# Performance work log

Hardware: AMD Instinct MI355X
Metric: run time of the kernel (lower is better)

Reference implementation:

```python
import jax, jax.numpy as jnp
import numpy as np

D = 64       # hidden_dim
ED = 16      # edge_dim
N = 50000
E = 400000
T = 2
STEP = 0.5   # euler fixed step over t in [0,1] -> 2 steps
EPS = 1e-5

def setup_inputs() -> dict:
    key = jax.random.key(0)
    ks = jax.random.split(key, 14)
    def lin(k, fi, fo):
        return jax.random.normal(k, (fi, fo), jnp.float32) / np.sqrt(fi)
    return {
        'h_seq': jax.random.normal(ks[0], (T, N, D), jnp.float32),
        'edge_attr': jax.random.normal(ks[1], (T, E, ED), jnp.float32),
        # msg_net: MLP(2D+ED -> D -> D), 2 layers with ReLU
        'W1': lin(ks[2], 2 * D + ED, D), 'b1': jnp.zeros((D,), jnp.float32),
        'W2': lin(ks[3], D, D),          'b2': jnp.zeros((D,), jnp.float32),
        # dynamics_net: Linear(2D,D) -> LayerNorm -> SiLU -> Linear(D,D) -> Tanh
        'Wd1': lin(ks[4], 2 * D, D), 'bd1': jnp.zeros((D,), jnp.float32),
        'ln_g': jnp.ones((D,), jnp.float32), 'ln_b': jnp.zeros((D,), jnp.float32),
        'Wd2': lin(ks[5], D, D), 'bd2': jnp.zeros((D,), jnp.float32),
        'edge_index': jax.random.randint(ks[6], (T, 2, E), 0, N, jnp.int32),
    }

def _ode_func(h, row, col, ea, W1, b1, W2, b2, Wd1, bd1, ln_g, ln_b, Wd2, bd2):
    # identity transport: Q_uv @ h_v == h_v
    h_transported = h[col]                              # [E, D]
    msg_in = jnp.concatenate([h[row], h_transported, ea], axis=-1)  # [E, 2D+ED]
    msg = jax.nn.relu(msg_in @ W1 + b1) @ W2 + b2       # [E, D]
    agg = jax.ops.segment_sum(msg, row, num_segments=h.shape[0])    # [N, D]
    x = jnp.concatenate([h, agg], axis=-1) @ Wd1 + bd1  # [N, D]
    mu = x.mean(-1, keepdims=True)
    var = x.var(-1, keepdims=True)
    x = (x - mu) * jax.lax.rsqrt(var + EPS) * ln_g + ln_b
    x = jax.nn.silu(x) @ Wd2 + bd2
    return jnp.tanh(x)

def reference(h_seq, edge_attr, W1, b1, W2, b2, Wd1, bd1, ln_g, ln_b, Wd2, bd2, edge_index):
    params = (W1, b1, W2, b2, Wd1, bd1, ln_g, ln_b, Wd2, bd2)
    n_steps = int(round(1.0 / STEP))
    h_prev = h_seq[0]
    disagreements = []
    for t in range(T):
        row, col = edge_index[t, 0], edge_index[t, 1]
        ea = edge_attr[t]
        h = h_prev + h_seq[t]                           # h_fused
        for _ in range(n_steps):                        # fixed-step Euler
            h = h + STEP * _ode_func(h, row, col, ea, *params)
        diff = h[row] - h[col]                          # Q=I -> h_u - h_v
        disagreements.append(jnp.minimum((diff * diff).sum(-1), 1e4))
        h_prev = h
    return h_prev, jnp.stack(disagreements)             # h_final [N,D], D [T,E]
```

## Files before the change

kernel.cpp:

```cpp
#include <hip/hip_runtime.h>

#define NN 50000
#define EE 400000
#define NT64 6250
#define EGRID 1250
#define NBLK 782
#define SBLK 49

typedef __bf16 bf16x8 __attribute__((ext_vector_type(8)));
typedef float f32x4 __attribute__((ext_vector_type(4)));

static __device__ __forceinline__ ushort f2bf(float f) {
    union { float f; unsigned int i; } x; x.f = f;
    unsigned int r = x.i + 0x7fffu + ((x.i >> 16) & 1u);
    return (ushort)(r >> 16);
}
static __device__ __forceinline__ float bf2f(ushort u) {
    union { unsigned int i; float f; } x; x.i = ((unsigned int)u) << 16; return x.f;
}
static __device__ __forceinline__ unsigned pack2(float lo, float hi) {
    return (unsigned)f2bf(lo) | ((unsigned)f2bf(hi) << 16);
}
static __device__ __forceinline__ float fast_tanh(float x) {
    float e = __expf(2.f * x);
    return 1.f - 2.f / (e + 1.f);
}
static __device__ __forceinline__ bf16x8 pk8(float4 f0, float4 f1) {
    union { uint4 u; bf16x8 v; } z;
    z.u = make_uint4(pack2(f0.x, f0.y), pack2(f0.z, f0.w),
                     pack2(f1.x, f1.y), pack2(f1.z, f1.w));
    return z.v;
}
static __device__ __forceinline__ bf16x8 zero8() {
    union { uint4 u; bf16x8 v; } z;
    z.u = make_uint4(0u, 0u, 0u, 0u);
    return z.v;
}

__global__ __launch_bounds__(256) void prep_edge_k(
    const float* __restrict__ W1, const float* __restrict__ W2,
    const float* __restrict__ b1, const float* __restrict__ b2,
    ushort* __restrict__ B1P, ushort* __restrict__ B2P,
    float* __restrict__ b1f, float* __restrict__ b2f)
{
    int idx = blockIdx.x * 256 + threadIdx.x;
    if (idx < 10240) {
        int j = idx & 7, n = (idx >> 3) & 63, qk = idx >> 9;
        int kc = qk >> 2, quad = qk & 3;
        int k = kc * 32 + quad * 8 + j;
        B1P[idx] = (k < 144) ? f2bf(W1[k * 64 + n]) : (ushort)0;
    }
    if (idx < 4096) {
        int j = idx & 7, n = (idx >> 3) & 63, qk = idx >> 9;
        int kc = qk >> 2, quad = qk & 3;
        int k = kc * 32 + quad * 8 + j;
        B2P[idx] = f2bf(W2[k * 64 + n]);
    }
    if (idx < 64) { b1f[idx] = b1[idx]; b2f[idx] = b2[idx]; }
}

__global__ __launch_bounds__(256) void prep_node_k(
    const float* __restrict__ Wd1, const float* __restrict__ Wd2,
    const float* __restrict__ bd1, const float* __restrict__ lng,
    const float* __restrict__ lnb, const float* __restrict__ bd2,
    ushort* __restrict__ Wd1P, ushort* __restrict__ Wd2P,
    float* __restrict__ bd1f, float* __restrict__ lngf,
    float* __restrict__ lnbf, float* __restrict__ bd2f)
{
    int idx = blockIdx.x * 256 + threadIdx.x;
    if (idx < 8192) {
        int j = idx & 7, n = (idx >> 3) & 63, qk = idx >> 9;
        int kc = qk >> 2, quad = qk & 3;
        int k = kc * 32 + quad * 8 + j;
        Wd1P[idx] = f2bf(Wd1[k * 64 + n]);
    }
    if (idx < 4096) {
        int j = idx & 7, n = (idx >> 3) & 63, qk = idx >> 9;
        int kc = qk >> 2, quad = qk & 3;
        int k = kc * 32 + quad * 8 + j;
        Wd2P[idx] = f2bf(Wd2[k * 64 + n]);
    }
    if (idx < 64) {
        bd1f[idx] = bd1[idx]; lngf[idx] = lng[idx];
        lnbf[idx] = lnb[idx]; bd2f[idx] = bd2[idx];
    }
}

__global__ __launch_bounds__(256) void state_k(
    float* __restrict__ h, ushort* __restrict__ hb,
    const float* __restrict__ hseq_t, int mode)
{
    int i = blockIdx.x * 256 + threadIdx.x;
    float v = hseq_t[i];
    float r = (mode == 0) ? (2.f * v) : (h[i] + v);
    h[i] = r; hb[i] = f2bf(r);
}

__global__ __launch_bounds__(256) void zero_k(int* __restrict__ p, int n) {
    int i = blockIdx.x * 256 + threadIdx.x;
    if (i < n) p[i] = 0;
}
__global__ __launch_bounds__(256) void zero_f(float* __restrict__ p) {
    int i = blockIdx.x * 256 + threadIdx.x;
    p[i] = 0.f;
}
__global__ __launch_bounds__(256) void hist_k(const int* __restrict__ ei, int* __restrict__ counts) {
    int e = blockIdx.x * 256 + threadIdx.x;
    const int* rows = ei + (size_t)blockIdx.y * 2 * EE;
    int* cnt = counts + blockIdx.y * NN;
    if (e < EE) atomicAdd(&cnt[rows[e]], 1);
}
__global__ __launch_bounds__(256) void scanA_k(
    const int* __restrict__ counts_, int* __restrict__ offsets_, int* __restrict__ bsum_)
{
    const int* counts = counts_ + blockIdx.y * NN;
    int* offsets = offsets_ + blockIdx.y * (NN + 1);
    int* bsum = bsum_ + blockIdx.y * 64;
    __shared__ int wsum[4];
    int tid = threadIdx.x, lane = tid & 63, w = tid >> 6;
    int i4 = blockIdx.x * 1024 + tid * 4;
    int4 v = make_int4(0, 0, 0, 0);
    if (i4 + 3 < NN) v = *(const int4*)(counts + i4);
    else {
        if (i4 < NN) v.x = counts[i4];
        if (i4 + 1 < NN) v.y = counts[i4 + 1];
        if (i4 + 2 < NN) v.z = counts[i4 + 2];
    }
    int s = v.x + v.y + v.z + v.w;
    int x = s;
    for (int off = 1; off < 64; off <<= 1) {
        int y = __shfl_up(x, off);
        if (lane >= off) x += y;
    }
    if (lane == 63) wsum[w] = x;
    __syncthreads();
    int wpre = 0;
    for (int j = 0; j < w; j++) wpre += wsum[j];
    int excl = wpre + x - s;
    int e0 = excl, e1 = e0 + v.x, e2 = e1 + v.y, e3 = e2 + v.z;
    if (i4 + 3 < NN) *(int4*)(offsets + i4) = make_int4(e0, e1, e2, e3);
    else {
        if (i4 < NN) offsets[i4] = e0;
        if (i4 + 1 < NN) offsets[i4 + 1] = e1;
        if (i4 + 2 < NN) offsets[i4 + 2] = e2;
    }
    if (tid == 255) bsum[blockIdx.x] = wpre + x;
}
__global__ __launch_bounds__(256) void scanC_k(
    int* __restrict__ offsets_, const int* __restrict__ bsum_, int* __restrict__ cursor_)
{
    int* offsets = offsets_ + blockIdx.y * (NN + 1);
    const int* bsum = bsum_ + blockIdx.y * 64;
    int* cursor = cursor_ + blockIdx.y * NN;
    int i = blockIdx.x * 256 + threadIdx.x;
    if (i < NN) {
        int b = i >> 10;
        int add = 0;
        for (int j = 0; j < b; j++) add += bsum[j];
        int o = offsets[i] + add;
        offsets[i] = o; cursor[i] = o;
    }
    if (i == 0) offsets[NN] = EE;
}
__global__ __launch_bounds__(256) void fill_idx_k(
    const int* __restrict__ ei, int* __restrict__ cursor_, int* __restrict__ esort_)
{
    int e = blockIdx.x * 256 + threadIdx.x;
    const int* rows = ei + (size_t)blockIdx.y * 2 * EE;
    int* cursor = cursor_ + blockIdx.y * NN;
    int* esort = esort_ + (size_t)blockIdx.y * EE;
    if (e < EE) {
        int p = atomicAdd(&cursor[rows[e]], 1);
        if ((unsigned)p < (unsigned)EE) esort[p] = e;
    }
}

__global__ __launch_bounds__(256) void gather_k(
    const int* __restrict__ esort, const int* __restrict__ rows,
    const int* __restrict__ cols, const float* __restrict__ ea,
    int* __restrict__ rsort, int* __restrict__ csort, ushort* __restrict__ eab)
{
    int p = blockIdx.x * 256 + threadIdx.x;
    if (p < EE) {
        int e = esort[p];
        rsort[p] = rows[e];
        csort[p] = cols[e];
        const float* sp = ea + (size_t)e * 16;
        float4 f0 = ((const float4*)sp)[0], f1 = ((const float4*)sp)[1];
        float4 f2 = ((const float4*)sp)[2], f3 = ((const float4*)sp)[3];
        uint4* dp = (uint4*)(eab + (size_t)p * 16);
        dp[0] = make_uint4(pack2(f0.x, f0.y), pack2(f0.z, f0.w),
                           pack2(f1.x, f1.y), pack2(f1.z, f1.w));
        dp[1] = make_uint4(pack2(f2.x, f2.y), pack2(f2.z, f2.w),
                           pack2(f3.x, f3.y), pack2(f3.z, f3.w));
    }
}

__global__ __launch_bounds__(256, 5) void edge_k(
    const ushort* __restrict__ hb,
    const int* __restrict__ ridx, const int* __restrict__ cidx,
    const ushort* __restrict__ eab,
    const ushort* __restrict__ B1P, const ushort* __restrict__ B2P,
    const float* __restrict__ b1f, const float* __restrict__ b2f,
    ushort* __restrict__ msg)
{
    __shared__ __attribute__((aligned(16))) ushort sB1[10240];
    __shared__ __attribute__((aligned(16))) ushort sH[64 * 72];

    int tid = threadIdx.x;
    int lane = tid & 63, wave = tid >> 6;
    int m = lane & 15, quad = lane >> 4;

    for (int i = tid; i < 10240 / 8; i += 256) ((uint4*)sB1)[i] = ((const uint4*)B1P)[i];
    bf16x8 b2r[2][4];
    for (int kc = 0; kc < 2; kc++)
        for (int nt = 0; nt < 4; nt++)
            b2r[kc][nt] = *(const bf16x8*)(B2P + ((kc * 4 + quad) * 64 + nt * 16 + m) * 8);
    float b1v[4], b2v[4];
    for (int nt = 0; nt < 4; nt++) { b1v[nt] = b1f[nt * 16 + m]; b2v[nt] = b2f[nt * 16 + m]; }
    __syncthreads();

    ushort* sHw = sH + wave * 1152;
    int sl = wave * 16 + m;
    int t0 = blockIdx.x * 5;

    int rc = ridx[t0 * 64 + sl], cc = cidx[t0 * 64 + sl];
    bf16x8 aC[5];
    aC[0] = *(const bf16x8*)(hb + (size_t)rc * 64 + quad * 8);
    aC[1] = *(const bf16x8*)(hb + (size_t)rc * 64 + 32 + quad * 8);
    aC[2] = *(const bf16x8*)(hb + (size_t)cc * 64 + quad * 8);
    aC[3] = *(const bf16x8*)(hb + (size_t)cc * 64 + 32 + quad * 8);
    aC[4] = zero8();
    if (quad < 2) aC[4] = *(const bf16x8*)(eab + (size_t)(t0 * 64 + sl) * 16 + quad * 8);
    int rn = ridx[(t0 + 1) * 64 + sl], cn = cidx[(t0 + 1) * 64 + sl];

    for (int t = t0; t < t0 + 5; t++) {
        int tn = (t + 1 < t0 + 5) ? t + 1 : t;
        bf16x8 aN[5];
        aN[0] = *(const bf16x8*)(hb + (size_t)rn * 64 + quad * 8);
        aN[1] = *(const bf16x8*)(hb + (size_t)rn * 64 + 32 + quad * 8);
        aN[2] = *(const bf16x8*)(hb + (size_t)cn * 64 + quad * 8);
        aN[3] = *(const bf16x8*)(hb + (size_t)cn * 64 + 32 + quad * 8);
        aN[4] = zero8();
        if (quad < 2) aN[4] = *(const bf16x8*)(eab + (size_t)(tn * 64 + sl) * 16 + quad * 8);
        int tnn = (t + 2 < t0 + 5) ? t + 2 : t;
        int rn2 = ridx[tnn * 64 + sl], cn2 = cidx[tnn * 64 + sl];

        f32x4 acc[4];
        #pragma unroll
        for (int nt = 0; nt < 4; nt++) acc[nt] = (f32x4){0.f, 0.f, 0.f, 0.f};
        #pragma unroll
        for (int kc = 0; kc < 5; kc++) {
            #pragma unroll
            for (int nt = 0; nt < 4; nt++) {
                bf16x8 b = *(const bf16x8*)(sB1 + ((kc * 4 + quad) * 64 + nt * 16 + m) * 8);
                acc[nt] = __builtin_amdgcn_mfma_f32_16x16x32_bf16(aC[kc], b, acc[nt], 0, 0, 0);
            }
        }

        __builtin_amdgcn_wave_barrier();
        #pragma unroll
        for (int nt = 0; nt < 4; nt++) {
            int colid = nt * 16 + m;
            float bb = b1v[nt];
            #pragma unroll
            for (int rr = 0; rr < 4; rr++) {
                float v = acc[nt][rr] + bb;
                v = v > 0.f ? v : 0.f;
                sHw[(quad * 4 + rr) * 72 + colid] = f2bf(v);
            }
        }
        __builtin_amdgcn_wave_barrier();

        f32x4 acc2[4];
        #pragma unroll
        for (int nt = 0; nt < 4; nt++) acc2[nt] = (f32x4){0.f, 0.f, 0.f, 0.f};
        #pragma unroll
        for (int kc = 0; kc < 2; kc++) {
            bf16x8 av = *(const bf16x8*)(sHw + m * 72 + kc * 32 + quad * 8);
            #pragma unroll
            for (int nt = 0; nt < 4; nt++) {
                acc2[nt] = __builtin_amdgcn_mfma_f32_16x16x32_bf16(av, b2r[kc][nt], acc2[nt], 0, 0, 0);
            }
        }

        #pragma unroll
        for (int nt = 0; nt < 4; nt++) {
            int colid = nt * 16 + m;
            float bb = b2v[nt];
            #pragma unroll
            for (int rr = 0; rr < 4; rr++) {
                int so = t * 64 + wave * 16 + quad * 4 + rr;
                msg[(size_t)so * 64 + colid] = f2bf(acc2[nt][rr] + bb);
            }
        }

        #pragma unroll
        for (int k2 = 0; k2 < 5; k2++) aC[k2] = aN[k2];
        rn = rn2; cn = cn2;
    }
}

__global__ __launch_bounds__(256, 5) void nodeagg_k(
    float* __restrict__ h, ushort* __restrict__ hbm,
    const ushort* __restrict__ msg, const int* __restrict__ offsets,
    const ushort* __restrict__ Wd1P, const ushort* __restrict__ Wd2P,
    const float* __restrict__ bd1f, const float* __restrict__ lngf,
    const float* __restrict__ lnbf, const float* __restrict__ bd2f)
{
    __shared__ __attribute__((aligned(16))) float aggL[64][68];
    __shared__ __attribute__((aligned(16))) ushort sX[64 * 72];
    int tid = threadIdx.x;
    int lane = tid & 63, wave = tid >> 6;
    int m = lane & 15, quad = lane >> 4;
    int nbase = blockIdx.x * 64;

    for (int idx = wave; idx < 64; idx += 4) {
        int n = nbase + idx;
        float a = 0.f;
        if (n < NN) {
            int bgn = offsets[n], end2 = offsets[n + 1];
            int i = bgn;
            for (; i + 4 <= end2; i += 4) {
                a += bf2f(msg[(size_t)i * 64 + lane]);
                a += bf2f(msg[(size_t)(i + 1) * 64 + lane]);
                a += bf2f(msg[(size_t)(i + 2) * 64 + lane]);
                a += bf2f(msg[(size_t)(i + 3) * 64 + lane]);
            }
            for (; i < end2; i++) a += bf2f(msg[(size_t)i * 64 + lane]);
        }
        aggL[idx][lane] = a;
    }

    float gA[4], bA[4], d1[4], d2[4];
    for (int nt = 0; nt < 4; nt++) {
        int f = nt * 16 + m;
        d1[nt] = bd1f[f]; gA[nt] = lngf[f]; bA[nt] = lnbf[f]; d2[nt] = bd2f[f];
    }
    __syncthreads();

    int n_true = nbase + wave * 16 + m;
    bool own = (n_true < NN);
    int n = own ? n_true : (NN - 1);
    int nl = wave * 16 + m;
    bf16x8 A[4];
    A[0] = *(const bf16x8*)(hbm + (size_t)n * 64 + quad * 8);
    A[1] = *(const bf16x8*)(hbm + (size_t)n * 64 + 32 + quad * 8);
    {
        float4 g0 = *(const float4*)&aggL[nl][quad * 8];
        float4 g1 = *(const float4*)&aggL[nl][quad * 8 + 4];
        float4 g2 = *(const float4*)&aggL[nl][32 + quad * 8];
        float4 g3 = *(const float4*)&aggL[nl][32 + quad * 8 + 4];
        A[2] = pk8(g0, g1);
        A[3] = pk8(g2, g3);
    }

    f32x4 acc[4];
    #pragma unroll
    for (int nt = 0; nt < 4; nt++) acc[nt] = (f32x4){0.f, 0.f, 0.f, 0.f};
    #pragma unroll
    for (int kc = 0; kc < 4; kc++) {
        #pragma unroll
        for (int nt = 0; nt < 4; nt++) {
            bf16x8 b = *(const bf16x8*)(Wd1P + ((kc * 4 + quad) * 64 + nt * 16 + m) * 8);
            acc[nt] = __builtin_amdgcn_mfma_f32_16x16x32_bf16(A[kc], b, acc[nt], 0, 0, 0);
        }
    }

    float xs[4][4];
    #pragma unroll
    for (int nt = 0; nt < 4; nt++)
        #pragma unroll
        for (int r = 0; r < 4; r++)
            xs[nt][r] = acc[nt][r] + d1[nt];

    ushort* sXw = sX + wave * 1152;
    #pragma unroll
    for (int r = 0; r < 4; r++) {
        float s1 = 0.f, s2 = 0.f;
        #pragma unroll
        for (int nt = 0; nt < 4; nt++) { float v = xs[nt][r]; s1 += v; s2 += v * v; }
        for (int off = 1; off < 16; off <<= 1) {
            s1 += __shfl_xor(s1, off);
            s2 += __shfl_xor(s2, off);
        }
        float mean = s1 * (1.f / 64.f);
        float var = fmaxf(s2 * (1.f / 64.f) - mean * mean, 0.f);
        float rstd = rsqrtf(var + 1e-5f);
        #pragma unroll
        for (int nt = 0; nt < 4; nt++) {
            float xn = (xs[nt][r] - mean) * rstd * gA[nt] + bA[nt];
            float slv = xn / (1.f + __expf(-xn));
            sXw[(quad * 4 + r) * 72 + nt * 16 + m] = f2bf(slv);
        }
    }
    __builtin_amdgcn_wave_barrier();

    f32x4 acc2[4];
    #pragma unroll
    for (int nt = 0; nt < 4; nt++) acc2[nt] = (f32x4){0.f, 0.f, 0.f, 0.f};
    #pragma unroll
    for (int kc = 0; kc < 2; kc++) {
        bf16x8 av = *(const bf16x8*)(sXw + m * 72 + kc * 32 + quad * 8);
        #pragma unroll
        for (int nt = 0; nt < 4; nt++) {
            bf16x8 b = *(const bf16x8*)(Wd2P + ((kc * 4 + quad) * 64 + nt * 16 + m) * 8);
            acc2[nt] = __builtin_amdgcn_mfma_f32_16x16x32_bf16(av, b, acc2[nt], 0, 0, 0);
        }
    }

    #pragma unroll
    for (int r = 0; r < 4; r++) {
        int g = nbase + wave * 16 + quad * 4 + r;
        if (g < NN) {
            #pragma unroll
            for (int nt = 0; nt < 4; nt++) {
                int f = nt * 16 + m;
                float y = fast_tanh(acc2[nt][r] + d2[nt]);
                float hn = h[(size_t)g * 64 + f] + 0.5f * y;
                h[(size_t)g * 64 + f] = hn;
                hbm[(size_t)g * 64 + f] = f2bf(hn);
            }
        }
    }
}

__global__ __launch_bounds__(256, 5) void edge_fb_k(
    const ushort* __restrict__ hb,
    const int* __restrict__ ridx, const int* __restrict__ cidx,
    const float* __restrict__ eaf,
    const ushort* __restrict__ B1P, const ushort* __restrict__ B2P,
    const float* __restrict__ b1f, const float* __restrict__ b2f,
    float* __restrict__ agg)
{
    __shared__ __attribute__((aligned(16))) ushort sB1[10240];
    __shared__ __attribute__((aligned(16))) ushort sH[64 * 72];

    int tid = threadIdx.x;
    int lane = tid & 63, wave = tid >> 6;
    int m = lane & 15, quad = lane >> 4;

    for (int i = tid; i < 10240 / 8; i += 256) ((uint4*)sB1)[i] = ((const uint4*)B1P)[i];
    bf16x8 b2r[2][4];
    for (int kc = 0; kc < 2; kc++)
        for (int nt = 0; nt < 4; nt++)
            b2r[kc][nt] = *(const bf16x8*)(B2P + ((kc * 4 + quad) * 64 + nt * 16 + m) * 8);
    float b1v[4], b2v[4];
    for (int nt = 0; nt < 4; nt++) { b1v[nt] = b1f[nt * 16 + m]; b2v[nt] = b2f[nt * 16 + m]; }
    __syncthreads();

    ushort* sHw = sH + wave * 1152;
    int sl = wave * 16 + m;
    int t0 = blockIdx.x * 5;

    for (int t = t0; t < t0 + 5; t++) {
        int s = t * 64 + sl;
        int r = ridx[s], c = cidx[s];
        bf16x8 a[5];
        a[0] = *(const bf16x8*)(hb + (size_t)r * 64 + quad * 8);
        a[1] = *(const bf16x8*)(hb + (size_t)r * 64 + 32 + quad * 8);
        a[2] = *(const bf16x8*)(hb + (size_t)c * 64 + quad * 8);
        a[3] = *(const bf16x8*)(hb + (size_t)c * 64 + 32 + quad * 8);
        a[4] = zero8();
        if (quad < 2) {
            const float* sp = eaf + (size_t)s * 16 + quad * 8;
            a[4] = pk8(((const float4*)sp)[0], ((const float4*)sp)[1]);
        }
        f32x4 acc[4];
        #pragma unroll
        for (int nt = 0; nt < 4; nt++) acc[nt] = (f32x4){0.f, 0.f, 0.f, 0.f};
        #pragma unroll
        for (int kc = 0; kc < 5; kc++)
            #pragma unroll
            for (int nt = 0; nt < 4; nt++) {
                bf16x8 b = *(const bf16x8*)(sB1 + ((kc * 4 + quad) * 64 + nt * 16 + m) * 8);
                acc[nt] = __builtin_amdgcn_mfma_f32_16x16x32_bf16(a[kc], b, acc[nt], 0, 0, 0);
            }
        __builtin_amdgcn_wave_barrier();
        #pragma unroll
        for (int nt = 0; nt < 4; nt++) {
            float bb = b1v[nt];
            #pragma unroll
            for (int rr = 0; rr < 4; rr++) {
                float v = acc[nt][rr] + bb;
                v = v > 0.f ? v : 0.f;
                sHw[(quad * 4 + rr) * 72 + nt * 16 + m] = f2bf(v);
            }
        }
        __builtin_amdgcn_wave_barrier();
        f32x4 acc2[4];
        #pragma unroll
        for (int nt = 0; nt < 4; nt++) acc2[nt] = (f32x4){0.f, 0.f, 0.f, 0.f};
        #pragma unroll
        for (int kc = 0; kc < 2; kc++) {
            bf16x8 av = *(const bf16x8*)(sHw + m * 72 + kc * 32 + quad * 8);
            #pragma unroll
            for (int nt = 0; nt < 4; nt++)
                acc2[nt] = __builtin_amdgcn_mfma_f32_16x16x32_bf16(av, b2r[kc][nt], acc2[nt], 0, 0, 0);
        }
        int base = t * 64 + wave * 16 + quad * 4;
        int r0 = ridx[base], r1 = ridx[base + 1], r2 = ridx[base + 2], r3 = ridx[base + 3];
        #pragma unroll
        for (int nt = 0; nt < 4; nt++) {
            int colid = nt * 16 + m;
            float bb = b2v[nt];
            float v0 = acc2[nt][0] + bb, v1 = acc2[nt][1] + bb;
            float v2 = acc2[nt][2] + bb, v3 = acc2[nt][3] + bb;
            float sum = v0; int pr = r0;
            if (r1 == pr) sum += v1;
            else { atomicAdd(&agg[(size_t)pr * 64 + colid], sum); pr = r1; sum = v1; }
            if (r2 == pr) sum += v2;
            else { atomicAdd(&agg[(size_t)pr * 64 + colid], sum); pr = r2; sum = v2; }
            if (r3 == pr) sum += v3;
            else { atomicAdd(&agg[(size_t)pr * 64 + colid], sum); pr = r3; sum = v3; }
            atomicAdd(&agg[(size_t)pr * 64 + colid], sum);
        }
    }
}

__global__ __launch_bounds__(256, 4) void node_k(
    float* __restrict__ h, ushort* __restrict__ hbm,
    float* __restrict__ agg,
    const ushort* __restrict__ Wd1P, const ushort* __restrict__ Wd2P,
    const float* __restrict__ bd1f, const float* __restrict__ lngf,
    const float* __restrict__ lnbf, const float* __restrict__ bd2f)
{
    __shared__ __attribute__((aligned(16))) ushort sB1[8192];
    __shared__ __attribute__((aligned(16))) ushort sB2[4096];
    __shared__ __attribute__((aligned(16))) ushort sX[64 * 72];
    int tid = threadIdx.x;
    int lane = tid & 63, wave = tid >> 6;
    int m = lane & 15, quad = lane >> 4;
    int nbase = blockIdx.x * 64;

    for (int i = tid; i < 8192 / 8; i += 256) ((uint4*)sB1)[i] = ((const uint4*)Wd1P)[i];
    for (int i = tid; i < 4096 / 8; i += 256) ((uint4*)sB2)[i] = ((const uint4*)Wd2P)[i];
    float gA[4], bA[4], d1[4], d2[4];
    for (int nt = 0; nt < 4; nt++) {
        int f = nt * 16 + m;
        d1[nt] = bd1f[f]; gA[nt] = lngf[f]; bA[nt] = lnbf[f]; d2[nt] = bd2f[f];
    }
    __syncthreads();

    int n_true = nbase + wave * 16 + m;
    bool own = (n_true < NN);
    int n = own ? n_true : (NN - 1);
    bf16x8 A[4];
    A[0] = *(const bf16x8*)(hbm + (size_t)n * 64 + quad * 8);
    A[1] = *(const bf16x8*)(hbm + (size_t)n * 64 + 32 + quad * 8);
    {
        const float* ap = agg + (size_t)n * 64 + quad * 8;
        float4 g0 = ((const float4*)ap)[0], g1 = ((const float4*)ap)[1];
        const float* ap2 = agg + (size_t)n * 64 + 32 + quad * 8;
        float4 g2 = ((const float4*)ap2)[0], g3 = ((const float4*)ap2)[1];
        A[2] = pk8(g0, g1);
        A[3] = pk8(g2, g3);
        if (own) {
            float4 z = make_float4(0.f, 0.f, 0.f, 0.f);
            ((float4*)(agg + (size_t)n * 64 + quad * 8))[0] = z;
            ((float4*)(agg + (size_t)n * 64 + quad * 8))[1] = z;
            ((float4*)(agg + (size_t)n * 64 + 32 + quad * 8))[0] = z;
            ((float4*)(agg + (size_t)n * 64 + 32 + quad * 8))[1] = z;
        }
    }

    f32x4 acc[4];
    #pragma unroll
    for (int nt = 0; nt < 4; nt++) acc[nt] = (f32x4){0.f, 0.f, 0.f, 0.f};
    #pragma unroll
    for (int kc = 0; kc < 4; kc++)
        #pragma unroll
        for (int nt = 0; nt < 4; nt++) {
            bf16x8 b = *(const bf16x8*)(sB1 + ((kc * 4 + quad) * 64 + nt * 16 + m) * 8);
            acc[nt] = __builtin_amdgcn_mfma_f32_16x16x32_bf16(A[kc], b, acc[nt], 0, 0, 0);
        }

    float xs[4][4];
    #pragma unroll
    for (int nt = 0; nt < 4; nt++)
        #pragma unroll
        for (int r = 0; r < 4; r++)
            xs[nt][r] = acc[nt][r] + d1[nt];

    ushort* sXw = sX + wave * 1152;
    #pragma unroll
    for (int r = 0; r < 4; r++) {
        float s1 = 0.f, s2 = 0.f;
        #pragma unroll
        for (int nt = 0; nt < 4; nt++) { float v = xs[nt][r]; s1 += v; s2 += v * v; }
        for (int off = 1; off < 16; off <<= 1) {
            s1 += __shfl_xor(s1, off);
            s2 += __shfl_xor(s2, off);
        }
        float mean = s1 * (1.f / 64.f);
        float var = fmaxf(s2 * (1.f / 64.f) - mean * mean, 0.f);
        float rstd = rsqrtf(var + 1e-5f);
        #pragma unroll
        for (int nt = 0; nt < 4; nt++) {
            float xn = (xs[nt][r] - mean) * rstd * gA[nt] + bA[nt];
            float slv = xn / (1.f + __expf(-xn));
            sXw[(quad * 4 + r) * 72 + nt * 16 + m] = f2bf(slv);
        }
    }
    __builtin_amdgcn_wave_barrier();

    f32x4 acc2[4];
    #pragma unroll
    for (int nt = 0; nt < 4; nt++) acc2[nt] = (f32x4){0.f, 0.f, 0.f, 0.f};
    #pragma unroll
    for (int kc = 0; kc < 2; kc++) {
        bf16x8 av = *(const bf16x8*)(sXw + m * 72 + kc * 32 + quad * 8);
        #pragma unroll
        for (int nt = 0; nt < 4; nt++) {
            bf16x8 b = *(const bf16x8*)(sB2 + ((kc * 4 + quad) * 64 + nt * 16 + m) * 8);
            acc2[nt] = __builtin_amdgcn_mfma_f32_16x16x32_bf16(av, b, acc2[nt], 0, 0, 0);
        }
    }

    #pragma unroll
    for (int r = 0; r < 4; r++) {
        int g = nbase + wave * 16 + quad * 4 + r;
        if (g < NN) {
            #pragma unroll
            for (int nt = 0; nt < 4; nt++) {
                int f = nt * 16 + m;
                float y = fast_tanh(acc2[nt][r] + d2[nt]);
                float hn = h[(size_t)g * 64 + f] + 0.5f * y;
                h[(size_t)g * 64 + f] = hn;
                hbm[(size_t)g * 64 + f] = f2bf(hn);
            }
        }
    }
}

__global__ __launch_bounds__(256) void dis_k(
    const float* __restrict__ h, const int* __restrict__ rows,
    const int* __restrict__ cols, float* __restrict__ outp)
{
    int tid = threadIdx.x;
    int e = blockIdx.x * 16 + (tid >> 4);
    int l16 = tid & 15;
    int r = rows[e], c = cols[e];
    float4 a = *(const float4*)(h + (size_t)r * 64 + l16 * 4);
    float4 b = *(const float4*)(h + (size_t)c * 64 + l16 * 4);
    float dx = a.x - b.x, dy = a.y - b.y, dz = a.z - b.z, dw = a.w - b.w;
    float s = dx * dx + dy * dy + dz * dz + dw * dw;
    for (int off = 1; off < 16; off <<= 1) s += __shfl_xor(s, off);
    if (l16 == 0) outp[e] = (s < 1e4f ? s : 1e4f);
}

__global__ __launch_bounds__(256) void final_k(const float* __restrict__ h, float* __restrict__ out) {
    int i = blockIdx.x * 256 + threadIdx.x;
    out[i] = h[i];
}

extern "C" void kernel_launch(void* const* d_in, const int* in_sizes, int n_in,
                              void* d_out, int out_size, void* d_ws, size_t ws_size,
                              hipStream_t stream) {
    const float* h_seq = (const float*)d_in[0];
    const float* eattr = (const float*)d_in[1];
    const float* W1 = (const float*)d_in[2];
    const float* b1 = (const float*)d_in[3];
    const float* W2 = (const float*)d_in[4];
    const float* b2 = (const float*)d_in[5];
    const float* Wd1 = (const float*)d_in[6];
    const float* bd1 = (const float*)d_in[7];
    const float* lng = (const float*)d_in[8];
    const float* lnb = (const float*)d_in[9];
    const float* Wd2 = (const float*)d_in[10];
    const float* bd2 = (const float*)d_in[11];
    const int* ei = (const int*)d_in[12];
    float* out = (float*)d_out;

    char* wsp = (char*)d_ws;
    size_t used = 0;
    auto carve = [&](size_t b) {
        void* p = (void*)(wsp + used);
        used += (b + 255) & ~(size_t)255;
        return p;
    };
    float* h0     = (float*)carve((size_t)NN * 64 * 4);
    ushort* hb0   = (ushort*)carve((size_t)NN * 64 * 2);
    float* agg    = (float*)carve((size_t)NN * 64 * 4);
    ushort* B1P   = (ushort*)carve(10240 * 2);
    ushort* B2P   = (ushort*)carve(4096 * 2);
    ushort* Wd1P  = (ushort*)carve(8192 * 2);
    ushort* Wd2P  = (ushort*)carve(4096 * 2);
    float* b1f    = (float*)carve(256);
    float* b2f    = (float*)carve(256);
    float* bd1f   = (float*)carve(256);
    float* lngf   = (float*)carve(256);
    float* lnbf   = (float*)carve(256);
    float* bd2f   = (float*)carve(256);
    int* counts   = (int*)carve((size_t)2 * NN * 4);
    int* offsets  = (int*)carve((size_t)2 * (NN + 1) * 4);
    int* cursor   = (int*)carve((size_t)2 * NN * 4);
    int* bsum     = (int*)carve(512);
    int* esort    = (int*)carve((size_t)2 * EE * 4);
    int* rsort    = (int*)carve((size_t)EE * 4);
    int* csort    = (int*)carve((size_t)EE * 4);
    ushort* eab   = (ushort*)carve((size_t)EE * 16 * 2);
    ushort* msg   = (ushort*)carve((size_t)EE * 64 * 2);
    const bool full = (used <= ws_size);

    prep_edge_k<<<40, 256, 0, stream>>>(W1, W2, b1, b2, B1P, B2P, b1f, b2f);
    prep_node_k<<<32, 256, 0, stream>>>(Wd1, Wd2, bd1, lng, lnb, bd2, Wd1P, Wd2P, bd1f, lngf, lnbf, bd2f);
    if (!full) zero_f<<<12500, 256, 0, stream>>>(agg);

    if (full) {
        zero_k<<<391, 256, 0, stream>>>(counts, 2 * NN);
        hist_k<<<dim3(1563, 2), 256, 0, stream>>>(ei, counts);
        scanA_k<<<dim3(SBLK, 2), 256, 0, stream>>>(counts, offsets, bsum);
        scanC_k<<<dim3(196, 2), 256, 0, stream>>>(offsets, bsum, cursor);
        fill_idx_k<<<dim3(1563, 2), 256, 0, stream>>>(ei, cursor, esort);
    }

    for (int t = 0; t < 2; t++) {
        const int* rows = ei + (size_t)t * 2 * EE;
        const int* cols = rows + EE;
        const float* eat = eattr + (size_t)t * EE * 16;
        state_k<<<12500, 256, 0, stream>>>(h0, hb0, h_seq + (size_t)t * NN * 64, t);
        if (full) {
            gather_k<<<1563, 256, 0, stream>>>(esort + (size_t)t * EE, rows, cols, eat,
                                               rsort, csort, eab);
            const int* offs_t = offsets + (size_t)t * (NN + 1);
            for (int s = 0; s < 2; s++) {
                edge_k<<<EGRID, 256, 0, stream>>>(hb0, rsort, csort, eab,
                                                  B1P, B2P, b1f, b2f, msg);
                nodeagg_k<<<NBLK, 256, 0, stream>>>(h0, hb0, msg, offs_t, Wd1P, Wd2P,
                                                    bd1f, lngf, lnbf, bd2f);
            }
        } else {
            for (int s = 0; s < 2; s++) {
                edge_fb_k<<<EGRID, 256, 0, stream>>>(hb0, rows, cols, eat,
                                                     B1P, B2P, b1f, b2f, agg);
                node_k<<<NBLK, 256, 0, stream>>>(h0, hb0, agg, Wd1P, Wd2P,
                                                 bd1f, lngf, lnbf, bd2f);
            }
        }
        dis_k<<<25000, 256, 0, stream>>>(h0, rows, cols, out + (size_t)NN * 64 + (size_t)t * EE);
    }
    final_k<<<12500, 256, 0, stream>>>(h0, out);
}
```

Before: 614.1 us.

## Scatter edge messages to sorted slots instead of pre-gathering sorted edge data

The gather kernel, which permuted row/col indices and bf16-converted edge attributes into row-sorted order, is removed. The edge kernel now reads edges in original order, converts fp32 edge attributes on the fly, and writes each message to its CSR slot using an inverse-permutation array built by fill_idx. This drops one pass over edge data per time step. In exchange, message writes become scattered rather than contiguous, and edge attributes are reloaded in fp32 on every Euler step.

```diff
diff --git a/kernel.cpp b/kernel.cpp
--- a/kernel.cpp
+++ b/kernel.cpp
@@ -163,43 +163,22 @@
     if (i == 0) offsets[NN] = EE;
 }
 __global__ __launch_bounds__(256) void fill_idx_k(
-    const int* __restrict__ ei, int* __restrict__ cursor_, int* __restrict__ esort_)
+    const int* __restrict__ ei, int* __restrict__ cursor_, int* __restrict__ eslot_)
 {
     int e = blockIdx.x * 256 + threadIdx.x;
     const int* rows = ei + (size_t)blockIdx.y * 2 * EE;
     int* cursor = cursor_ + blockIdx.y * NN;
-    int* esort = esort_ + (size_t)blockIdx.y * EE;
+    int* eslot = eslot_ + (size_t)blockIdx.y * EE;
     if (e < EE) {
         int p = atomicAdd(&cursor[rows[e]], 1);
-        if ((unsigned)p < (unsigned)EE) esort[p] = e;
-    }
-}
-
-__global__ __launch_bounds__(256) void gather_k(
-    const int* __restrict__ esort, const int* __restrict__ rows,
-    const int* __restrict__ cols, const float* __restrict__ ea,
-    int* __restrict__ rsort, int* __restrict__ csort, ushort* __restrict__ eab)
-{
-    int p = blockIdx.x * 256 + threadIdx.x;
-    if (p < EE) {
-        int e = esort[p];
-        rsort[p] = rows[e];
-        csort[p] = cols[e];
-        const float* sp = ea + (size_t)e * 16;
-        float4 f0 = ((const float4*)sp)[0], f1 = ((const float4*)sp)[1];
-        float4 f2 = ((const float4*)sp)[2], f3 = ((const float4*)sp)[3];
-        uint4* dp = (uint4*)(eab + (size_t)p * 16);
-        dp[0] = make_uint4(pack2(f0.x, f0.y), pack2(f0.z, f0.w),
-                           pack2(f1.x, f1.y), pack2(f1.z, f1.w));
-        dp[1] = make_uint4(pack2(f2.x, f2.y), pack2(f2.z, f2.w),
-                           pack2(f3.x, f3.y), pack2(f3.z, f3.w));
+        eslot[e] = ((unsigned)p < (unsigned)EE) ? p : 0;
     }
 }
 
 __global__ __launch_bounds__(256, 5) void edge_k(
     const ushort* __restrict__ hb,
-    const int* __restrict__ ridx, const int* __restrict__ cidx,
-    const ushort* __restrict__ eab,
+    const int* __restrict__ rows, const int* __restrict__ cols,
+    const float* __restrict__ eaf, const int* __restrict__ eslot,
     const ushort* __restrict__ B1P, const ushort* __restrict__ B2P,
     const float* __restrict__ b1f, const float* __restrict__ b2f,
     ushort* __restrict__ msg)
@@ -224,15 +203,18 @@
     int sl = wave * 16 + m;
     int t0 = blockIdx.x * 5;
 
-    int rc = ridx[t0 * 64 + sl], cc = cidx[t0 * 64 + sl];
+    int rc = rows[t0 * 64 + sl], cc = cols[t0 * 64 + sl];
     bf16x8 aC[5];
     aC[0] = *(const bf16x8*)(hb + (size_t)rc * 64 + quad * 8);
     aC[1] = *(const bf16x8*)(hb + (size_t)rc * 64 + 32 + quad * 8);
     aC[2] = *(const bf16x8*)(hb + (size_t)cc * 64 + quad * 8);
     aC[3] = *(const bf16x8*)(hb + (size_t)cc * 64 + 32 + quad * 8);
     aC[4] = zero8();
-    if (quad < 2) aC[4] = *(const bf16x8*)(eab + (size_t)(t0 * 64 + sl) * 16 + quad * 8);
-    int rn = ridx[(t0 + 1) * 64 + sl], cn = cidx[(t0 + 1) * 64 + sl];
+    if (quad < 2) {
+        const float* sp = eaf + (size_t)(t0 * 64 + sl) * 16 + quad * 8;
+        aC[4] = pk8(((const float4*)sp)[0], ((const float4*)sp)[1]);
+    }
+    int rn = rows[(t0 + 1) * 64 + sl], cn = cols[(t0 + 1) * 64 + sl];
 
     for (int t = t0; t < t0 + 5; t++) {
         int tn = (t + 1 < t0 + 5) ? t + 1 : t;
@@ -242,9 +224,12 @@
         aN[2] = *(const bf16x8*)(hb + (size_t)cn * 64 + quad * 8);
         aN[3] = *(const bf16x8*)(hb + (size_t)cn * 64 + 32 + quad * 8);
         aN[4] = zero8();
-        if (quad < 2) aN[4] = *(const bf16x8*)(eab + (size_t)(tn * 64 + sl) * 16 + quad * 8);
+        if (quad < 2) {
+            const float* sp = eaf + (size_t)(tn * 64 + sl) * 16 + quad * 8;
+            aN[4] = pk8(((const float4*)sp)[0], ((const float4*)sp)[1]);
+        }
         int tnn = (t + 2 < t0 + 5) ? t + 2 : t;
-        int rn2 = ridx[tnn * 64 + sl], cn2 = cidx[tnn * 64 + sl];
+        int rn2 = rows[tnn * 64 + sl], cn2 = cols[tnn * 64 + sl];
 
         f32x4 acc[4];
         #pragma unroll
@@ -284,15 +269,17 @@
             }
         }
 
+        int base = t * 64 + wave * 16 + quad * 4;
+        int4 p4 = *(const int4*)(eslot + base);
+        int ps0 = p4.x, ps1 = p4.y, ps2 = p4.z, ps3 = p4.w;
         #pragma unroll
         for (int nt = 0; nt < 4; nt++) {
             int colid = nt * 16 + m;
             float bb = b2v[nt];
-            #pragma unroll
-            for (int rr = 0; rr < 4; rr++) {
-                int so = t * 64 + wave * 16 + quad * 4 + rr;
-                msg[(size_t)so * 64 + colid] = f2bf(acc2[nt][rr] + bb);
-            }
+            msg[(size_t)ps0 * 64 + colid] = f2bf(acc2[nt][0] + bb);
+            msg[(size_t)ps1 * 64 + colid] = f2bf(acc2[nt][1] + bb);
+            msg[(size_t)ps2 * 64 + colid] = f2bf(acc2[nt][2] + bb);
+            msg[(size_t)ps3 * 64 + colid] = f2bf(acc2[nt][3] + bb);
         }
 
         #pragma unroll
@@ -696,10 +683,7 @@
     int* offsets  = (int*)carve((size_t)2 * (NN + 1) * 4);
     int* cursor   = (int*)carve((size_t)2 * NN * 4);
     int* bsum     = (int*)carve(512);
-    int* esort    = (int*)carve((size_t)2 * EE * 4);
-    int* rsort    = (int*)carve((size_t)EE * 4);
-    int* csort    = (int*)carve((size_t)EE * 4);
-    ushort* eab   = (ushort*)carve((size_t)EE * 16 * 2);
+    int* eslot    = (int*)carve((size_t)2 * EE * 4);
     ushort* msg   = (ushort*)carve((size_t)EE * 64 * 2);
     const bool full = (used <= ws_size);
 
@@ -712,7 +696,7 @@
         hist_k<<<dim3(1563, 2), 256, 0, stream>>>(ei, counts);
         scanA_k<<<dim3(SBLK, 2), 256, 0, stream>>>(counts, offsets, bsum);
         scanC_k<<<dim3(196, 2), 256, 0, stream>>>(offsets, bsum, cursor);
-        fill_idx_k<<<dim3(1563, 2), 256, 0, stream>>>(ei, cursor, esort);
+        fill_idx_k<<<dim3(1563, 2), 256, 0, stream>>>(ei, cursor, eslot);
     }
 
     for (int t = 0; t < 2; t++) {
@@ -721,11 +705,10 @@
         const float* eat = eattr + (size_t)t * EE * 16;
         state_k<<<12500, 256, 0, stream>>>(h0, hb0, h_seq + (size_t)t * NN * 64, t);
         if (full) {
-            gather_k<<<1563, 256, 0, stream>>>(esort + (size_t)t * EE, rows, cols, eat,
-                                               rsort, csort, eab);
             const int* offs_t = offsets + (size_t)t * (NN + 1);
+            const int* eslot_t = eslot + (size_t)t * EE;
             for (int s = 0; s < 2; s++) {
-                edge_k<<<EGRID, 256, 0, stream>>>(hb0, rsort, csort, eab,
+                edge_k<<<EGRID, 256, 0, stream>>>(hb0, rows, cols, eat, eslot_t,
                                                   B1P, B2P, b1f, b2f, msg);
                 nodeagg_k<<<NBLK, 256, 0, stream>>>(h0, hb0, msg, offs_t, Wd1P, Wd2P,
                                                     bd1f, lngf, lnbf, bd2f);
```

Measured after the change: 626.7 us. +2.1%, slower.
